# Optimization experiments

Hardware: AMD Instinct MI355X
Metric: run time of the kernel (lower is better)

Reference implementation:

```python
import jax, jax.numpy as jnp
import numpy as np
from jax import lax


def setup_inputs() -> dict:
    key = jax.random.key(0)
    k1, k2 = jax.random.split(key)
    B, C, H, W = 8, 16, 128, 128
    rate = 2
    hs = H // rate
    hw = hs * hs
    x = jax.random.normal(k1, (B, C, H, W), dtype=jnp.float32)
    scores = jax.random.normal(k2, (B, hw, hw), dtype=jnp.float32)
    alpha = jnp.ones((1,), dtype=jnp.float32)
    return {"x": x, "scores": scores, "alpha": alpha}


def reference(x, scores, alpha):
    B, C, H, W = x.shape
    P = scores.shape[2]              # hw = hs*ws
    hs = int(np.sqrt(P))
    ws = hs
    rate = H // hs
    vk = 2 * rate                    # vksize
    pad = rate // 2                  # vpadding (ReplicationPad2d)

    # --- extract_patches: replication pad + unfold(kernel=vk, stride=rate) ---
    xp = jnp.pad(x, ((0, 0), (0, 0), (pad, pad), (pad, pad)), mode='edge')
    ii = (jnp.arange(hs) * rate)[:, None] + jnp.arange(vk)[None, :]   # [hs, vk]
    jj = (jnp.arange(ws) * rate)[:, None] + jnp.arange(vk)[None, :]   # [ws, vk]
    # gather overlapping patches: [B, C, hs, vk, ws, vk]
    V = xp[:, :, ii][:, :, :, :, jj]
    # -> [B, hs*ws, C, vk, vk] matching torch layout (B, hs, ws, C, vk, vk)
    V = V.transpose(0, 2, 4, 1, 3, 5).reshape(B, hs * ws, C, vk, vk)

    # --- scores: permute(0,2,1) then reshape to per-patch spatial maps ---
    S = scores.transpose(0, 2, 1).reshape(B, P, hs, ws)  # channel p = key index

    # --- grouped conv_transpose2d(stride=rate, padding=pad, groups=B) ---
    # torch conv_transpose2d == lhs-dilated conv with flipped, transposed kernel
    # and padding (vk - 1 - pad) per side; vmapped over batch (one group each).
    w_pad = vk - 1 - pad

    def conv_t(s, v):
        # s: [P, hs, ws] (input channels = patches); v: [P, C, vk, vk]
        w = jnp.flip(v, axis=(-2, -1)).transpose(1, 0, 2, 3)  # [C, P, vk, vk]
        out = lax.conv_general_dilated(
            s[None], w,
            window_strides=(1, 1),
            padding=[(w_pad, w_pad), (w_pad, w_pad)],
            lhs_dilation=(rate, rate),
            dimension_numbers=('NCHW', 'OIHW', 'NCHW'))
        return out[0]  # [C, H, W]

    y = jax.vmap(conv_t)(S, V) / 4.0  # [B, C, H, W]
    return x + y * alpha
```

## Files before the change

### kernel.cpp

```cpp
#include <hip/hip_runtime.h>
#include <hip/hip_bf16.h>

typedef float f32x4 __attribute__((ext_vector_type(4)));
typedef short bf16x8 __attribute__((ext_vector_type(8)));
typedef unsigned short us8 __attribute__((ext_vector_type(8)));
typedef unsigned short us4 __attribute__((ext_vector_type(4)));

__device__ __forceinline__ unsigned short f2bf(float f) {
  union { float f; unsigned u; } v; v.f = f;
  return (unsigned short)((v.u + 0x8000u) >> 16);
}
__device__ __forceinline__ float bf2f(unsigned short u) {
  union { unsigned u; float f; } v; v.u = ((unsigned)u) << 16;
  return v.f;
}

__global__ __launch_bounds__(256) void prep_vmat(const float* __restrict__ x,
                                                 unsigned short* __restrict__ vmatT) {
  int t = blockIdx.x * 256 + threadIdx.x;
  int pc = t & 511;
  int n  = (t >> 9) & 255;
  int b  = t >> 17;
  int c = n >> 4, u = (n >> 2) & 3, v = n & 3;
  int pi = pc >> 3;
  int pj0 = (pc & 7) << 3;
  int row = 2 * pi + u - 1;
  row = row < 0 ? 0 : (row > 127 ? 127 : row);
  const float* xr = x + ((size_t)(b * 16 + c) * 128 + row) * 128;
  us8 o;
#pragma unroll
  for (int e = 0; e < 8; ++e) {
    int col = 2 * (pj0 + e) + v - 1;
    col = col < 0 ? 0 : (col > 127 ? 127 : col);
    o[e] = f2bf(xr[col]);
  }
  *reinterpret_cast<us8*>(vmatT + (size_t)t * 8) = o;
}

__global__ __launch_bounds__(512, 2) void gemm_scores_vmat(
    const float* __restrict__ scores,
    const unsigned short* __restrict__ vmatT,
    unsigned short* __restrict__ Amat) {
  __shared__ unsigned short ldsB[4][16384];

  int bid = blockIdx.x;
  int batch = bid & 7;
  int qb = (bid >> 3) << 7;
  const int phase = ((bid >> 3) * 2) & 63;

  const int t = threadIdx.x;
  const int lane = t & 63;
  const int wq = t >> 6;
  const int l15 = lane & 15, l16 = lane >> 4;

  const float* aLane =
      scores + ((size_t)(batch * 4096 + qb + wq * 16 + l15)) * 4096 + l16 * 8;
  const unsigned short* Vb = vmatT + (size_t)batch * 256 * 4096;

  const unsigned short* bSrc[4];
#pragma unroll
  for (int i = 0; i < 4; ++i) {
    int c = t + i * 512;
    int gs = (c & 7) ^ ((c >> 3) & 7);
    bSrc[i] = Vb + (size_t)(c >> 3) * 4096 + gs * 8;
  }
  const int pos0 = (l16 ^ (l15 & 7)) << 3;

  f32x4 acc[16];
#pragma unroll
  for (int ni = 0; ni < 16; ++ni) acc[ni] = (f32x4){0.f, 0.f, 0.f, 0.f};

  f32x4 r0[4], r1[4], r2[4], r3[4];
  bf16x8 fa0, fa1;

#define SB __builtin_amdgcn_sched_barrier(0)
#define STAGE_B(kt, bufi)                                                     \
  {                                                                           \
    int kp_ = ((kt) + phase) & 63;                                            \
    _Pragma("unroll") for (int i = 0; i < 4; ++i)                             \
        __builtin_amdgcn_global_load_lds(                                     \
            (const __attribute__((address_space(1))) void*)(bSrc[i] + (size_t)kp_ * 64), \
            (__attribute__((address_space(3))) void*)&ldsB[bufi][(t + i * 512) * 8], \
            16, 0, 0);                                                        \
  }
#define LOAD_A(kt, rr)                                                        \
  {                                                                           \
    int kp_ = ((kt) + phase) & 63;                                            \
    const float* ap_ = aLane + (size_t)kp_ * 64;                              \
    rr[0] = *(const f32x4*)(ap_);                                             \
    rr[1] = *(const f32x4*)(ap_ + 4);                                         \
    rr[2] = *(const f32x4*)(ap_ + 32);                                        \
    rr[3] = *(const f32x4*)(ap_ + 36);                                        \
  }
#define CONV(rr)                                                              \
  {                                                                           \
    _Pragma("unroll") for (int e = 0; e < 4; ++e) {                           \
      fa0[e] = (short)f2bf(rr[0][e]); fa0[e + 4] = (short)f2bf(rr[1][e]);     \
      fa1[e] = (short)f2bf(rr[2][e]); fa1[e + 4] = (short)f2bf(rr[3][e]);     \
    }                                                                         \
  }
#define MFMAS(bufi)                                                           \
  {                                                                           \
    _Pragma("unroll") for (int ni = 0; ni < 16; ++ni) {                       \
      bf16x8 bv = *(const bf16x8*)(&ldsB[bufi][0] +                           \
                                   (ni * 16 + l15) * 64 + pos0);              \
      acc[ni] = __builtin_amdgcn_mfma_f32_16x16x32_bf16(fa0, bv, acc[ni],     \
                                                        0, 0, 0);             \
    }                                                                         \
    _Pragma("unroll") for (int ni = 0; ni < 16; ++ni) {                       \
      bf16x8 bv = *(const bf16x8*)(&ldsB[bufi][0] +                           \
                                   (ni * 16 + l15) * 64 + (pos0 ^ 32));      \
      acc[ni] = __builtin_amdgcn_mfma_f32_16x16x32_bf16(fa1, bv, acc[ni],     \
                                                        0, 0, 0);             \
    }                                                                         \
  }
#define BODY(m, kt, rr)                                                       \
  {                                                                           \
    CONV(rr);                                                                 \
    SB;                                                                       \
    STAGE_B((kt) + 2, ((m) + 2) & 3);                                         \
    SB;                                                                       \
    LOAD_A((kt) + 4, rr);                                                     \
    SB;                                                                       \
    MFMAS(m);                                                                 \
    SB;                                                                       \
    asm volatile("s_waitcnt vmcnt(12)" ::: "memory");                         \
    SB;                                                                       \
    __builtin_amdgcn_s_barrier();                                             \
    SB;                                                                       \
  }

  STAGE_B(0, 0);
  SB;
  LOAD_A(0, r0);
  SB;
  LOAD_A(1, r1);
  SB;
  LOAD_A(2, r2);
  SB;
  STAGE_B(1, 1);
  SB;
  LOAD_A(3, r3);
  SB;
  asm volatile("s_waitcnt vmcnt(12)" ::: "memory");
  SB;
  __builtin_amdgcn_s_barrier();
  SB;

  for (int kt = 0; kt < 64; kt += 4) {
    BODY(0, kt, r0);
    BODY(1, kt + 1, r1);
    BODY(2, kt + 2, r2);
    BODY(3, kt + 3, r3);
  }

  asm volatile("" ::"v"(r0[0][0]), "v"(r1[0][0]), "v"(r2[0][0]), "v"(r3[0][0]),
               "v"(r0[3][0]), "v"(r1[3][0]), "v"(r2[3][0]), "v"(r3[3][0]));

#undef SB
#undef STAGE_B
#undef LOAD_A
#undef CONV
#undef MFMAS
#undef BODY

  unsigned short* Ao = Amat + ((size_t)(batch * 4096 + qb + wq * 16)) * 256;
#pragma unroll
  for (int ni = 0; ni < 16; ++ni)
#pragma unroll
    for (int j = 0; j < 4; ++j)
      Ao[(size_t)(l16 * 4 + j) * 256 + ni * 16 + l15] = f2bf(acc[ni][j]);
}

__global__ __launch_bounds__(256) void epilogue_kernel(
    const float* __restrict__ x, const unsigned short* __restrict__ Amat,
    const float* __restrict__ alpha, float* __restrict__ out) {
  __shared__ unsigned short L[2 * 64 * 66];

  int b = blockIdx.x >> 7;
  int h = blockIdx.x & 127;
  int t = threadIdx.x;

  int ihi = (h + 1) >> 1, u_hi = (h + 1) & 1;
  bool p0ok = (ihi <= 63), p1ok = (ihi >= 1);
  const unsigned short* Ab = Amat + (size_t)b * 4096 * 256;

  unsigned int* Lw = reinterpret_cast<unsigned int*>(L);
#pragma unroll
  for (int p = 0; p < 2; ++p) {
    bool ok = p ? p1ok : p0ok;
    int rbase = (p ? (ihi - 1) : ihi) * 64;
    int u = u_hi + 2 * p;
#pragma unroll
    for (int i = 0; i < 4; ++i) {
      int q = t + 256 * i;
      int j = q >> 4, c = q & 15;
      us4 ch = (us4){0, 0, 0, 0};
      if (ok)
        ch = *reinterpret_cast<const us4*>(Ab + (size_t)(rbase + j) * 256 +
                                           c * 16 + u * 4);
      int widx = (p * 4224 + j * 66 + c * 4) >> 1;
      Lw[widx]     = (unsigned int)(unsigned short)ch[0] |
                     ((unsigned int)(unsigned short)ch[1] << 16);
      Lw[widx + 1] = (unsigned int)(unsigned short)ch[2] |
                     ((unsigned int)(unsigned short)ch[3] << 16);
    }
  }
  __syncthreads();

  int w = t & 127;
  int cg = t >> 7;
  int jhi = (w + 1) >> 1, v_hi = (w + 1) & 1;
  bool vj_hi = (jhi <= 63), vj_lo = (jhi >= 1);
  float al = alpha[0] * 0.25f;

#pragma unroll
  for (int cc = 0; cc < 8; ++cc) {
    int c = cg * 8 + cc;
    float s = 0.f;
    if (vj_hi) {
      int o = jhi * 66 + c * 4 + v_hi;
      s += bf2f(L[o]) + bf2f(L[4224 + o]);
    }
    if (vj_lo) {
      int o = (jhi - 1) * 66 + c * 4 + v_hi + 2;
      s += bf2f(L[o]) + bf2f(L[4224 + o]);
    }
    size_t xi = (((size_t)b * 16 + c) * 128 + h) * 128 + w;
    out[xi] = x[xi] + al * s;
  }
}

extern "C" void kernel_launch(void* const* d_in, const int* in_sizes, int n_in,
                              void* d_out, int out_size, void* d_ws, size_t ws_size,
                              hipStream_t stream) {
  const float* x      = (const float*)d_in[0];
  const float* scores = (const float*)d_in[1];
  const float* alpha  = (const float*)d_in[2];
  float* out = (float*)d_out;

  unsigned short* vmatT = (unsigned short*)d_ws;
  unsigned short* Amat  = (unsigned short*)((char*)d_ws + (size_t)16 * 1024 * 1024);

  prep_vmat<<<4096, 256, 0, stream>>>(x, vmatT);
  gemm_scores_vmat<<<256, 512, 0, stream>>>(scores, vmatT, Amat);
  epilogue_kernel<<<1024, 256, 0, stream>>>(x, Amat, alpha, out);
}
```

Baseline: 162.4 us.

## Double K-tile to 128 with two-stage LDS buffering in scores GEMM

The K step per iteration grows from 64 to 128, and the LDS ring drops from four 64-wide buffers to two 128-wide buffers. A-operand prefetch goes from four register sets to two, and the swizzle is widened to 16 groups. This halves the number of barriers and waitcnt points per K loop, amortizing synchronization cost. In exchange it reduces pipeline depth, so load latency is hidden over fewer stages, and per-thread register pressure for A prefetch stays similar.

```diff
diff --git a/kernel.cpp b/kernel.cpp
--- a/kernel.cpp
+++ b/kernel.cpp
@@ -41,12 +41,12 @@
     const float* __restrict__ scores,
     const unsigned short* __restrict__ vmatT,
     unsigned short* __restrict__ Amat) {
-  __shared__ unsigned short ldsB[4][16384];
+  __shared__ unsigned short ldsB[2][32768];
 
   int bid = blockIdx.x;
   int batch = bid & 7;
   int qb = (bid >> 3) << 7;
-  const int phase = ((bid >> 3) * 2) & 63;
+  const int phase = (bid >> 3) & 31;
 
   const int t = threadIdx.x;
   const int lane = t & 63;
@@ -57,74 +57,74 @@
       scores + ((size_t)(batch * 4096 + qb + wq * 16 + l15)) * 4096 + l16 * 8;
   const unsigned short* Vb = vmatT + (size_t)batch * 256 * 4096;
 
-  const unsigned short* bSrc[4];
-#pragma unroll
-  for (int i = 0; i < 4; ++i) {
+  const unsigned short* bSrc[8];
+#pragma unroll
+  for (int i = 0; i < 8; ++i) {
     int c = t + i * 512;
-    int gs = (c & 7) ^ ((c >> 3) & 7);
-    bSrc[i] = Vb + (size_t)(c >> 3) * 4096 + gs * 8;
-  }
-  const int pos0 = (l16 ^ (l15 & 7)) << 3;
+    int gs = (c & 15) ^ ((c >> 4) & 15);
+    bSrc[i] = Vb + (size_t)(c >> 4) * 4096 + gs * 8;
+  }
 
   f32x4 acc[16];
 #pragma unroll
   for (int ni = 0; ni < 16; ++ni) acc[ni] = (f32x4){0.f, 0.f, 0.f, 0.f};
 
-  f32x4 r0[4], r1[4], r2[4], r3[4];
-  bf16x8 fa0, fa1;
+  f32x4 rE[8], rO[8];
+  bf16x8 fa[4];
 
 #define SB __builtin_amdgcn_sched_barrier(0)
 #define STAGE_B(kt, bufi)                                                     \
   {                                                                           \
-    int kp_ = ((kt) + phase) & 63;                                            \
-    _Pragma("unroll") for (int i = 0; i < 4; ++i)                             \
+    int kp_ = ((kt) + phase) & 31;                                            \
+    _Pragma("unroll") for (int i = 0; i < 8; ++i)                             \
         __builtin_amdgcn_global_load_lds(                                     \
-            (const __attribute__((address_space(1))) void*)(bSrc[i] + (size_t)kp_ * 64), \
+            (const __attribute__((address_space(1))) void*)(bSrc[i] + (size_t)kp_ * 128), \
             (__attribute__((address_space(3))) void*)&ldsB[bufi][(t + i * 512) * 8], \
             16, 0, 0);                                                        \
   }
 #define LOAD_A(kt, rr)                                                        \
   {                                                                           \
-    int kp_ = ((kt) + phase) & 63;                                            \
-    const float* ap_ = aLane + (size_t)kp_ * 64;                              \
+    int kp_ = ((kt) + phase) & 31;                                            \
+    const float* ap_ = aLane + (size_t)kp_ * 128;                             \
     rr[0] = *(const f32x4*)(ap_);                                             \
     rr[1] = *(const f32x4*)(ap_ + 4);                                         \
     rr[2] = *(const f32x4*)(ap_ + 32);                                        \
     rr[3] = *(const f32x4*)(ap_ + 36);                                        \
+    rr[4] = *(const f32x4*)(ap_ + 64);                                        \
+    rr[5] = *(const f32x4*)(ap_ + 68);                                        \
+    rr[6] = *(const f32x4*)(ap_ + 96);                                        \
+    rr[7] = *(const f32x4*)(ap_ + 100);                                       \
   }
 #define CONV(rr)                                                              \
   {                                                                           \
-    _Pragma("unroll") for (int e = 0; e < 4; ++e) {                           \
-      fa0[e] = (short)f2bf(rr[0][e]); fa0[e + 4] = (short)f2bf(rr[1][e]);     \
-      fa1[e] = (short)f2bf(rr[2][e]); fa1[e + 4] = (short)f2bf(rr[3][e]);     \
+    _Pragma("unroll") for (int f = 0; f < 4; ++f)                             \
+        _Pragma("unroll") for (int e = 0; e < 4; ++e) {                       \
+      fa[f][e]     = (short)f2bf(rr[2 * f][e]);                               \
+      fa[f][e + 4] = (short)f2bf(rr[2 * f + 1][e]);                           \
     }                                                                         \
   }
 #define MFMAS(bufi)                                                           \
   {                                                                           \
-    _Pragma("unroll") for (int ni = 0; ni < 16; ++ni) {                       \
+    _Pragma("unroll") for (int ks = 0; ks < 4; ++ks)                          \
+        _Pragma("unroll") for (int ni = 0; ni < 16; ++ni) {                   \
+      int pos = ((ks * 4 + l16) ^ l15) << 3;                                  \
       bf16x8 bv = *(const bf16x8*)(&ldsB[bufi][0] +                           \
-                                   (ni * 16 + l15) * 64 + pos0);              \
-      acc[ni] = __builtin_amdgcn_mfma_f32_16x16x32_bf16(fa0, bv, acc[ni],     \
+                                   (ni * 16 + l15) * 128 + pos);              \
+      acc[ni] = __builtin_amdgcn_mfma_f32_16x16x32_bf16(fa[ks], bv, acc[ni],  \
                                                         0, 0, 0);             \
     }                                                                         \
-    _Pragma("unroll") for (int ni = 0; ni < 16; ++ni) {                       \
-      bf16x8 bv = *(const bf16x8*)(&ldsB[bufi][0] +                           \
-                                   (ni * 16 + l15) * 64 + (pos0 ^ 32));      \
-      acc[ni] = __builtin_amdgcn_mfma_f32_16x16x32_bf16(fa1, bv, acc[ni],     \
-                                                        0, 0, 0);             \
-    }                                                                         \
-  }
-#define BODY(m, kt, rr)                                                       \
-  {                                                                           \
-    CONV(rr);                                                                 \
-    SB;                                                                       \
-    STAGE_B((kt) + 2, ((m) + 2) & 3);                                         \
-    SB;                                                                       \
-    LOAD_A((kt) + 4, rr);                                                     \
-    SB;                                                                       \
-    MFMAS(m);                                                                 \
-    SB;                                                                       \
-    asm volatile("s_waitcnt vmcnt(12)" ::: "memory");                         \
+  }
+#define BODY(b_, kt, rr)                                                      \
+  {                                                                           \
+    CONV(rr);                                      \
+    SB;                                                                       \
+    STAGE_B((kt) + 1, (b_) ^ 1);                                              \
+    SB;                                                                       \
+    LOAD_A((kt) + 2, rr);                                                     \
+    SB;                                                                       \
+    MFMAS(b_);                                                                \
+    SB;                                                                       \
+    asm volatile("s_waitcnt vmcnt(8)" ::: "memory");                          \
     SB;                                                                       \
     __builtin_amdgcn_s_barrier();                                             \
     SB;                                                                       \
@@ -132,30 +132,22 @@
 
   STAGE_B(0, 0);
   SB;
-  LOAD_A(0, r0);
-  SB;
-  LOAD_A(1, r1);
-  SB;
-  LOAD_A(2, r2);
-  SB;
-  STAGE_B(1, 1);
-  SB;
-  LOAD_A(3, r3);
-  SB;
-  asm volatile("s_waitcnt vmcnt(12)" ::: "memory");
+  LOAD_A(0, rE);
+  SB;
+  LOAD_A(1, rO);
+  SB;
+  asm volatile("s_waitcnt vmcnt(8)" ::: "memory");
   SB;
   __builtin_amdgcn_s_barrier();
   SB;
 
-  for (int kt = 0; kt < 64; kt += 4) {
-    BODY(0, kt, r0);
-    BODY(1, kt + 1, r1);
-    BODY(2, kt + 2, r2);
-    BODY(3, kt + 3, r3);
-  }
-
-  asm volatile("" ::"v"(r0[0][0]), "v"(r1[0][0]), "v"(r2[0][0]), "v"(r3[0][0]),
-               "v"(r0[3][0]), "v"(r1[3][0]), "v"(r2[3][0]), "v"(r3[3][0]));
+  for (int kt = 0; kt < 32; kt += 2) {
+    BODY(0, kt, rE);
+    BODY(1, kt + 1, rO);
+  }
+
+  asm volatile("" ::"v"(rE[0][0]), "v"(rE[3][0]), "v"(rE[5][0]), "v"(rE[7][0]),
+               "v"(rO[0][0]), "v"(rO[3][0]), "v"(rO[5][0]), "v"(rO[7][0]));
 
 #undef SB
 #undef STAGE_B
```

Measured after the change: 164.3 us. No clear change (+1.2%).

## Stage scores tile through swizzled LDS with triple-buffered B pipeline

Applied to the files above, without the earlier changes.

The GEMM kernel now converts the fp32 scores tile to bf16 cooperatively and writes it into a swizzled, double-buffered LDS region. Each wave then reads its A fragments from LDS instead of converting values held in registers per lane. The B operand moves from four to three LDS buffers, and the prefetch depth for A drops from four tiles to two. This is meant to cut register pressure and make the global loads of scores more coalesced, at the cost of extra LDS writes and reads plus an lgkmcnt wait in every iteration. The K-loop phase offset per block also changes.

```diff
diff --git a/kernel.cpp b/kernel.cpp
--- a/kernel.cpp
+++ b/kernel.cpp
@@ -41,12 +41,13 @@
     const float* __restrict__ scores,
     const unsigned short* __restrict__ vmatT,
     unsigned short* __restrict__ Amat) {
-  __shared__ unsigned short ldsB[4][16384];
+  __shared__ unsigned short ldsA[2][8192];
+  __shared__ unsigned short ldsB[3][16384];
 
   int bid = blockIdx.x;
   int batch = bid & 7;
   int qb = (bid >> 3) << 7;
-  const int phase = ((bid >> 3) * 2) & 63;
+  const int phase = (bid >> 3) & 63;
 
   const int t = threadIdx.x;
   const int lane = t & 63;
@@ -54,15 +55,18 @@
   const int l15 = lane & 15, l16 = lane >> 4;
 
   const float* aLane =
-      scores + ((size_t)(batch * 4096 + qb + wq * 16 + l15)) * 4096 + l16 * 8;
+      scores + ((size_t)(batch * 4096 + qb + (t >> 4))) * 4096 + (t & 15) * 4;
+  const int aW = ((((t & 15) >> 1) ^ ((t >> 4) & 7)) << 3) + (t & 1) * 4;
+
   const unsigned short* Vb = vmatT + (size_t)batch * 256 * 4096;
-
   const unsigned short* bSrc[4];
+  int bDst[4];
 #pragma unroll
   for (int i = 0; i < 4; ++i) {
     int c = t + i * 512;
     int gs = (c & 7) ^ ((c >> 3) & 7);
     bSrc[i] = Vb + (size_t)(c >> 3) * 4096 + gs * 8;
+    bDst[i] = c * 8;
   }
   const int pos0 = (l16 ^ (l15 & 7)) << 3;
 
@@ -70,97 +74,101 @@
 #pragma unroll
   for (int ni = 0; ni < 16; ++ni) acc[ni] = (f32x4){0.f, 0.f, 0.f, 0.f};
 
-  f32x4 r0[4], r1[4], r2[4], r3[4];
-  bf16x8 fa0, fa1;
+  f32x4 rE[4], rO[4];
 
 #define SB __builtin_amdgcn_sched_barrier(0)
-#define STAGE_B(kt, bufi)                                                     \
+#define STAGE_B(kt, sl)                                                       \
   {                                                                           \
     int kp_ = ((kt) + phase) & 63;                                            \
     _Pragma("unroll") for (int i = 0; i < 4; ++i)                             \
         __builtin_amdgcn_global_load_lds(                                     \
             (const __attribute__((address_space(1))) void*)(bSrc[i] + (size_t)kp_ * 64), \
-            (__attribute__((address_space(3))) void*)&ldsB[bufi][(t + i * 512) * 8], \
+            (__attribute__((address_space(3))) void*)&ldsB[sl][bDst[i]],      \
             16, 0, 0);                                                        \
   }
 #define LOAD_A(kt, rr)                                                        \
   {                                                                           \
     int kp_ = ((kt) + phase) & 63;                                            \
-    const float* ap_ = aLane + (size_t)kp_ * 64;                              \
-    rr[0] = *(const f32x4*)(ap_);                                             \
-    rr[1] = *(const f32x4*)(ap_ + 4);                                         \
-    rr[2] = *(const f32x4*)(ap_ + 32);                                        \
-    rr[3] = *(const f32x4*)(ap_ + 36);                                        \
-  }
-#define CONV(rr)                                                              \
-  {                                                                           \
-    _Pragma("unroll") for (int e = 0; e < 4; ++e) {                           \
-      fa0[e] = (short)f2bf(rr[0][e]); fa0[e + 4] = (short)f2bf(rr[1][e]);     \
-      fa1[e] = (short)f2bf(rr[2][e]); fa1[e + 4] = (short)f2bf(rr[3][e]);     \
+    _Pragma("unroll") for (int i = 0; i < 4; ++i)                             \
+        rr[i] = *(const f32x4*)(aLane + (size_t)i * 32 * 4096 +               \
+                                (size_t)kp_ * 64);                            \
+  }
+#define CONVW(rr, sl)                                                         \
+  {                                                                           \
+    _Pragma("unroll") for (int i = 0; i < 4; ++i) {                           \
+      us4 p;                                                                  \
+      _Pragma("unroll") for (int e = 0; e < 4; ++e) p[e] = f2bf(rr[i][e]);    \
+      *(us4*)&ldsA[sl][((t >> 4) + 32 * i) * 64 + aW] = p;                    \
     }                                                                         \
   }
-#define MFMAS(bufi)                                                           \
-  {                                                                           \
-    _Pragma("unroll") for (int ni = 0; ni < 16; ++ni) {                       \
-      bf16x8 bv = *(const bf16x8*)(&ldsB[bufi][0] +                           \
-                                   (ni * 16 + l15) * 64 + pos0);              \
-      acc[ni] = __builtin_amdgcn_mfma_f32_16x16x32_bf16(fa0, bv, acc[ni],     \
-                                                        0, 0, 0);             \
+#define MFMAS(sa, sb)                                                         \
+  {                                                                           \
+    _Pragma("unroll") for (int ks = 0; ks < 2; ++ks) {                        \
+      bf16x8 af = *(const bf16x8*)(&ldsA[sa][0] + (wq * 16 + l15) * 64 +      \
+                                   (((ks * 4 + l16) ^ (l15 & 7)) << 3));      \
+      _Pragma("unroll") for (int ni = 0; ni < 16; ++ni) {                     \
+        bf16x8 bv = *(const bf16x8*)(&ldsB[sb][0] + (ni * 16 + l15) * 64 +    \
+                                     (pos0 ^ (ks * 32)));                     \
+        acc[ni] = __builtin_amdgcn_mfma_f32_16x16x32_bf16(af, bv, acc[ni],    \
+                                                          0, 0, 0);           \
+      }                                                                       \
     }                                                                         \
-    _Pragma("unroll") for (int ni = 0; ni < 16; ++ni) {                       \
-      bf16x8 bv = *(const bf16x8*)(&ldsB[bufi][0] +                           \
-                                   (ni * 16 + l15) * 64 + (pos0 ^ 32));      \
-      acc[ni] = __builtin_amdgcn_mfma_f32_16x16x32_bf16(fa1, bv, acc[ni],     \
-                                                        0, 0, 0);             \
-    }                                                                         \
-  }
-#define BODY(m, kt, rr)                                                       \
-  {                                                                           \
-    CONV(rr);                                                                 \
-    SB;                                                                       \
-    STAGE_B((kt) + 2, ((m) + 2) & 3);                                         \
-    SB;                                                                       \
-    LOAD_A((kt) + 4, rr);                                                     \
-    SB;                                                                       \
-    MFMAS(m);                                                                 \
-    SB;                                                                       \
-    asm volatile("s_waitcnt vmcnt(12)" ::: "memory");                         \
+  }
+#define BODY(kt, cs, aslW, sbSt, ls, aslR, sbRd)                              \
+  {                                                                           \
+    CONVW(cs, aslW);                                                          \
+    SB;                                                                       \
+    STAGE_B((kt) + 2, sbSt);                                                  \
+    SB;                                                                       \
+    LOAD_A((kt) + 2, ls);                                                     \
+    SB;                                                                       \
+    MFMAS(aslR, sbRd);                                                        \
+    SB;                                                                       \
+    asm volatile("s_waitcnt lgkmcnt(0)" ::: "memory");                        \
+    asm volatile("s_waitcnt vmcnt(8)" ::: "memory");                          \
     SB;                                                                       \
     __builtin_amdgcn_s_barrier();                                             \
     SB;                                                                       \
   }
 
+  LOAD_A(0, rE);
+  SB;
   STAGE_B(0, 0);
   SB;
-  LOAD_A(0, r0);
-  SB;
-  LOAD_A(1, r1);
-  SB;
-  LOAD_A(2, r2);
+  LOAD_A(1, rO);
+  SB;
+  asm volatile("s_waitcnt vmcnt(8)" ::: "memory");
+  SB;
+  CONVW(rE, 0);
   SB;
   STAGE_B(1, 1);
   SB;
-  LOAD_A(3, r3);
-  SB;
-  asm volatile("s_waitcnt vmcnt(12)" ::: "memory");
+  asm volatile("s_waitcnt lgkmcnt(0)" ::: "memory");
+  asm volatile("s_waitcnt vmcnt(4)" ::: "memory");
   SB;
   __builtin_amdgcn_s_barrier();
   SB;
 
-  for (int kt = 0; kt < 64; kt += 4) {
-    BODY(0, kt, r0);
-    BODY(1, kt + 1, r1);
-    BODY(2, kt + 2, r2);
-    BODY(3, kt + 3, r3);
-  }
-
-  asm volatile("" ::"v"(r0[0][0]), "v"(r1[0][0]), "v"(r2[0][0]), "v"(r3[0][0]),
-               "v"(r0[3][0]), "v"(r1[3][0]), "v"(r2[3][0]), "v"(r3[3][0]));
+  for (int kt = 0; kt < 60; kt += 6) {
+    BODY(kt + 0, rO, 1, 2, rE, 0, 0);
+    BODY(kt + 1, rE, 0, 0, rO, 1, 1);
+    BODY(kt + 2, rO, 1, 1, rE, 0, 2);
+    BODY(kt + 3, rE, 0, 2, rO, 1, 0);
+    BODY(kt + 4, rO, 1, 0, rE, 0, 1);
+    BODY(kt + 5, rE, 0, 1, rO, 1, 2);
+  }
+  BODY(60, rO, 1, 2, rE, 0, 0);
+  BODY(61, rE, 0, 0, rO, 1, 1);
+  BODY(62, rO, 1, 1, rE, 0, 2);
+  BODY(63, rE, 0, 2, rO, 1, 0);
+
+  asm volatile("" ::"v"(rE[0][0]), "v"(rE[1][0]), "v"(rE[2][0]), "v"(rE[3][0]),
+               "v"(rO[0][0]), "v"(rO[1][0]), "v"(rO[2][0]), "v"(rO[3][0]));
 
 #undef SB
 #undef STAGE_B
 #undef LOAD_A
-#undef CONV
+#undef CONVW
 #undef MFMAS
 #undef BODY
 
```

Measured after the change: 165.6 us. 2.0% more time.
